# Performance work log

Hardware: AMD Instinct MI355X
Metric: run time of the kernel (lower is better)

The kernel has to match this reference:

```python
import jax, jax.numpy as jnp
import numpy as np

N_NODES = 100000
N_EDGES = 1600000
DIM_IN = 165
DIM_HID = 128


def setup_inputs() -> dict:
    key = jax.random.key(0)
    ks = jax.random.split(key, 8)
    x = jax.random.normal(ks[0], (N_NODES, DIM_IN), dtype=jnp.float32)
    edge_index = jax.random.randint(ks[1], (2, N_EDGES), 0, N_NODES, dtype=jnp.int64)
    s1 = 1.0 / np.sqrt(DIM_IN)
    s2 = 1.0 / np.sqrt(DIM_HID)
    # PyG GraphConv: lin_rel (with bias) applied to aggregated neighbors,
    # lin_root (no bias) applied to self features.
    W_rel1 = jax.random.uniform(ks[2], (DIM_HID, DIM_IN), jnp.float32, -s1, s1)
    b_rel1 = jax.random.uniform(ks[3], (DIM_HID,), jnp.float32, -s1, s1)
    W_root1 = jax.random.uniform(ks[4], (DIM_HID, DIM_IN), jnp.float32, -s1, s1)
    W_rel2 = jax.random.uniform(ks[5], (1, DIM_HID), jnp.float32, -s2, s2)
    b_rel2 = jax.random.uniform(ks[6], (1,), jnp.float32, -s2, s2)
    W_root2 = jax.random.uniform(ks[7], (1, DIM_HID), jnp.float32, -s2, s2)
    return {"x": x, "edge_index": edge_index,
            "W_rel1": W_rel1, "b_rel1": b_rel1, "W_root1": W_root1,
            "W_rel2": W_rel2, "b_rel2": b_rel2, "W_root2": W_root2}


def _graph_conv(x, src, dst, W_rel, b_rel, W_root):
    # agg[i] = sum_{(j->i) in E} x[j]  (add aggregation, source_to_target flow)
    agg = jax.ops.segment_sum(x[src], dst, num_segments=N_NODES)
    return agg @ W_rel.T + b_rel + x @ W_root.T


def reference(x, edge_index, W_rel1, b_rel1, W_root1, W_rel2, b_rel2, W_root2):
    src, dst = edge_index[0], edge_index[1]
    h = _graph_conv(x, src, dst, W_rel1, b_rel1, W_root1)
    h = jax.nn.relu(h)
    # dropout p=0.1 is identity in eval mode (deterministic reference)
    out = _graph_conv(h, src, dst, W_rel2, b_rel2, W_root2)
    return jax.nn.sigmoid(out)  # [N_NODES, 1]
```

## Files before the change

kernel.cpp:

```cpp
#include <hip/hip_runtime.h>
#include <hip/hip_bf16.h>
#include <math.h>

#define N_NODES 100000
#define N_EDGES 1600000
#define DIM_IN 165
#define DIM_HID 128
#define K_PAD 192
#define NBUCK 391
#define EPB 16384
#define NHB 98
#define CAP 6144

typedef __attribute__((ext_vector_type(8))) short short8v;
typedef __attribute__((ext_vector_type(4))) float f32x4;

__global__ void k_detect(const int* __restrict__ e32, int* __restrict__ flag,
                         int* __restrict__ gcount) {
    int t = threadIdx.x;
    if (t == 0) {
        int z = 0;
        for (int k = 0; k < 16; ++k) z |= e32[2 * k + 1];
        flag[0] = (z == 0) ? 1 : 0;
    }
    if (t < NBUCK) gcount[t] = 0;
}

__global__ void k_histB(const int* __restrict__ e32, const int* __restrict__ flag,
                        int* __restrict__ gcount, int* __restrict__ blockBase) {
    __shared__ int lc[NBUCK];
    int t = threadIdx.x;
    for (int i = t; i < NBUCK; i += 256) lc[i] = 0;
    __syncthreads();
    int isI64 = flag[0];
    int base = blockIdx.x * EPB;
    int lim = base + EPB; if (lim > N_EDGES) lim = N_EDGES;
    const long long* e64 = (const long long*)e32;
    for (int i = base + t; i < lim; i += 256) {
        int d = isI64 ? (int)e64[N_EDGES + i] : e32[N_EDGES + i];
        atomicAdd(&lc[d >> 8], 1);
    }
    __syncthreads();
    for (int b = t; b < NBUCK; b += 256)
        blockBase[blockIdx.x * NBUCK + b] = atomicAdd(&gcount[b], lc[b]);
}

__global__ void k_scanb(const int* __restrict__ gcount, int* __restrict__ bucketStart,
                        int* __restrict__ row_ptr) {
    __shared__ int s[512];
    int t = threadIdx.x;
    s[t] = (t < NBUCK) ? gcount[t] : 0;
    __syncthreads();
    for (int o = 1; o < 512; o <<= 1) {
        int v = s[t]; int a = (t >= o) ? s[t - o] : 0;
        __syncthreads(); s[t] = v + a; __syncthreads();
    }
    if (t < NBUCK) bucketStart[t + 1] = s[t];
    if (t == 0) { bucketStart[0] = 0; row_ptr[N_NODES] = N_EDGES; }
}

__global__ void k_scatterB(const int* __restrict__ e32, const int* __restrict__ flag,
                           const int* __restrict__ bucketStart, const int* __restrict__ blockBase,
                           int2* __restrict__ pairs) {
    __shared__ int lcur[NBUCK];
    int t = threadIdx.x;
    for (int b = t; b < NBUCK; b += 256)
        lcur[b] = bucketStart[b] + blockBase[blockIdx.x * NBUCK + b];
    __syncthreads();
    int isI64 = flag[0];
    int base = blockIdx.x * EPB;
    int lim = base + EPB; if (lim > N_EDGES) lim = N_EDGES;
    const long long* e64 = (const long long*)e32;
    for (int i = base + t; i < lim; i += 256) {
        int s, d;
        if (isI64) { s = (int)e64[i]; d = (int)e64[N_EDGES + i]; }
        else       { s = e32[i];      d = e32[N_EDGES + i]; }
        int pos = atomicAdd(&lcur[d >> 8], 1);
        pairs[pos] = make_int2(s, d);
    }
}

__global__ void k_sortB(const int2* __restrict__ pairs, const int* __restrict__ bucketStart,
                        int* __restrict__ row_ptr, int* __restrict__ esrc) {
    __shared__ int srcb[CAP];
    __shared__ int cnt[256];
    __shared__ int scn[256];
    int t = threadIdx.x;
    int b = blockIdx.x;
    int s0 = bucketStart[b], s1 = bucketStart[b + 1];
    int n = s1 - s0; if (n > CAP) n = CAP;
    cnt[t] = 0;
    __syncthreads();
    for (int i = t; i < n; i += 256) {
        int2 p = pairs[s0 + i];
        int ld = p.y & 255;
        srcb[i] = p.x | (ld << 20);
        atomicAdd(&cnt[ld], 1);
    }
    __syncthreads();
    scn[t] = cnt[t];
    __syncthreads();
    for (int o = 1; o < 256; o <<= 1) {
        int v = scn[t]; int a = (t >= o) ? scn[t - o] : 0;
        __syncthreads(); scn[t] = v + a; __syncthreads();
    }
    int excl = scn[t] - cnt[t];
    int node = b * 256 + t;
    if (node < N_NODES) row_ptr[node] = s0 + excl;
    __syncthreads();
    cnt[t] = excl;
    __syncthreads();
    for (int i = t; i < n; i += 256) {
        int v = srcb[i];
        int ld = v >> 20;
        int r = atomicAdd(&cnt[ld], 1);
        esrc[s0 + r] = v & 0xFFFFF;
    }
}

__global__ void k_prepw(const float* __restrict__ Wrel1, const float* __restrict__ Wroot1,
                        unsigned short* __restrict__ Wpk) {
    int idx = blockIdx.x * 256 + threadIdx.x;
    if (idx < (K_PAD / 8) * 256 * 8) {
        int j = idx & 7;
        int n = (idx >> 3) & 255;
        int p = idx >> 11;
        int k = p * 8 + j;
        float v = 0.f;
        if (k < DIM_IN) v = (n < 128) ? Wrel1[n * DIM_IN + k] : Wroot1[(n - 128) * DIM_IN + k];
        unsigned u = __float_as_uint(v);
        u += 0x7FFFu + ((u >> 16) & 1u);
        Wpk[idx] = (unsigned short)(u >> 16);
    }
}

__launch_bounds__(256, 4)
__global__ void k_gemm_mfma(const float* __restrict__ x, const unsigned short* __restrict__ Wpk,
                            unsigned short* __restrict__ y_rel, float* __restrict__ y_root) {
    __shared__ unsigned short lh[32][232];
    __shared__ unsigned short ll[32][232];
    int tid = threadIdx.x;
    int base = blockIdx.x * 32;

    const float4* xg = (const float4*)(x + (size_t)base * DIM_IN);
    for (int i = tid; i < 1320; i += 256) {
        float4 v = xg[i];
        int fi = i * 4;
        #pragma unroll
        for (int e = 0; e < 4; ++e) {
            int idx = fi + e;
            int r = idx / DIM_IN;
            int k = idx - r * DIM_IN;
            float f = (e == 0) ? v.x : (e == 1) ? v.y : (e == 2) ? v.z : v.w;
            unsigned u = __float_as_uint(f);
            unsigned short hi = (unsigned short)(u >> 16);
            float fhi = __uint_as_float(u & 0xFFFF0000u);
            float lo = f - fhi;
            unsigned short lob = (unsigned short)(__float_as_uint(lo) >> 16);
            lh[r][k] = hi;
            ll[r][k] = lob;
        }
    }
    for (int i = tid; i < 32 * (K_PAD - DIM_IN); i += 256) {
        int r = i / (K_PAD - DIM_IN);
        int k = DIM_IN + (i - r * (K_PAD - DIM_IN));
        lh[r][k] = 0; ll[r][k] = 0;
    }
    __syncthreads();

    int w = tid >> 6, l = tid & 63;
    int rowg = w & 1;
    int colh = w >> 1;
    int m = l & 15, kg = l >> 4;
    int arow = rowg * 16 + m;

    f32x4 acc[8];
    #pragma unroll
    for (int t = 0; t < 8; ++t) acc[t] = (f32x4){0.f, 0.f, 0.f, 0.f};

    const short8v* ap_h = (const short8v*)(&lh[arow][0]);
    const short8v* ap_l = (const short8v*)(&ll[arow][0]);
    const short8v* bp   = (const short8v*)Wpk;
    int bidx = kg * 256 + colh * 128 + m;

    #pragma unroll
    for (int kc = 0; kc < 6; ++kc) {
        short8v ah = ap_h[kc * 4 + kg];
        short8v al = ap_l[kc * 4 + kg];
        short8v bfrag[8];
        #pragma unroll
        for (int t = 0; t < 8; ++t) bfrag[t] = bp[bidx + kc * 1024 + t * 16];
        #pragma unroll
        for (int t = 0; t < 8; ++t)
            acc[t] = __builtin_amdgcn_mfma_f32_16x16x32_bf16(ah, bfrag[t], acc[t], 0, 0, 0);
        #pragma unroll
        for (int t = 0; t < 8; ++t)
            acc[t] = __builtin_amdgcn_mfma_f32_16x16x32_bf16(al, bfrag[t], acc[t], 0, 0, 0);
    }

    int orow = base + rowg * 16 + kg * 4;
    if (colh == 0) {
        #pragma unroll
        for (int t = 0; t < 8; ++t) {
            #pragma unroll
            for (int q = 0; q < 4; ++q) {
                unsigned u = __float_as_uint(acc[t][q]);
                u += 0x7FFFu + ((u >> 16) & 1u);
                y_rel[(size_t)(orow + q) * 128 + t * 16 + m] = (unsigned short)(u >> 16);
            }
        }
    } else {
        #pragma unroll
        for (int t = 0; t < 8; ++t) {
            #pragma unroll
            for (int q = 0; q < 4; ++q)
                y_root[(size_t)(orow + q) * 128 + t * 16 + m] = acc[t][q];
        }
    }
}

__launch_bounds__(256, 8)
__global__ void k_agg(const unsigned short* __restrict__ y_rel, const float* __restrict__ y_root,
                      const int* __restrict__ row_ptr, const int* __restrict__ esrc,
                      const float* __restrict__ b_rel1, const float* __restrict__ W_rel2,
                      const float* __restrict__ W_root2,
                      float* __restrict__ s_out, float* __restrict__ r_out) {
    int node = blockIdx.x * 4 + (threadIdx.x >> 6);
    int lane = threadIdx.x & 63;
    int li = lane & 15;
    int qid = lane >> 4;
    const uint4* yr = (const uint4*)y_rel;

    int e0 = row_ptr[node], e1 = row_ptr[node + 1];
    float a0 = 0.f, a1 = 0.f, a2 = 0.f, a3 = 0.f;
    float a4 = 0.f, a5 = 0.f, a6 = 0.f, a7 = 0.f;

    for (int eb = e0; eb < e1; eb += 64) {
        int cnt = e1 - eb; if (cnt > 64) cnt = 64;
        int ed = (eb + lane < e1) ? esrc[eb + lane] : 0;
        int kfull = cnt & ~3;
        for (int k = 0; k < kfull; k += 4) {
            int src = __shfl(ed, k + qid);
            uint4 v = yr[(size_t)src * 16 + li];
            a0 += __uint_as_float(v.x << 16); a1 += __uint_as_float(v.x & 0xFFFF0000u);
            a2 += __uint_as_float(v.y << 16); a3 += __uint_as_float(v.y & 0xFFFF0000u);
            a4 += __uint_as_float(v.z << 16); a5 += __uint_as_float(v.z & 0xFFFF0000u);
            a6 += __uint_as_float(v.w << 16); a7 += __uint_as_float(v.w & 0xFFFF0000u);
        }
        if (kfull < cnt) {
            int src = __shfl(ed, (kfull + qid < cnt) ? (kfull + qid) : kfull);
            if (kfull + qid < cnt) {
                uint4 v = yr[(size_t)src * 16 + li];
                a0 += __uint_as_float(v.x << 16); a1 += __uint_as_float(v.x & 0xFFFF0000u);
                a2 += __uint_as_float(v.y << 16); a3 += __uint_as_float(v.y & 0xFFFF0000u);
                a4 += __uint_as_float(v.z << 16); a5 += __uint_as_float(v.z & 0xFFFF0000u);
                a6 += __uint_as_float(v.w << 16); a7 += __uint_as_float(v.w & 0xFFFF0000u);
            }
        }
    }
    #pragma unroll
    for (int o = 16; o <= 32; o <<= 1) {
        a0 += __shfl_xor(a0, o); a1 += __shfl_xor(a1, o);
        a2 += __shfl_xor(a2, o); a3 += __shfl_xor(a3, o);
        a4 += __shfl_xor(a4, o); a5 += __shfl_xor(a5, o);
        a6 += __shfl_xor(a6, o); a7 += __shfl_xor(a7, o);
    }

    const float4* bb = (const float4*)(b_rel1 + 8 * li);
    const float4* rt = (const float4*)(y_root + (size_t)node * 128 + 8 * li);
    const float4* w2 = (const float4*)(W_rel2 + 8 * li);
    const float4* wo = (const float4*)(W_root2 + 8 * li);
    float4 b0 = bb[0], b1 = bb[1];
    float4 r0 = rt[0], r1 = rt[1];
    float4 p0 = w2[0], p1 = w2[1];
    float4 q0 = wo[0], q1 = wo[1];
    float h0 = fmaxf(a0 + b0.x + r0.x, 0.f), h1 = fmaxf(a1 + b0.y + r0.y, 0.f);
    float h2 = fmaxf(a2 + b0.z + r0.z, 0.f), h3 = fmaxf(a3 + b0.w + r0.w, 0.f);
    float h4 = fmaxf(a4 + b1.x + r1.x, 0.f), h5 = fmaxf(a5 + b1.y + r1.y, 0.f);
    float h6 = fmaxf(a6 + b1.z + r1.z, 0.f), h7 = fmaxf(a7 + b1.w + r1.w, 0.f);
    float sd = h0 * p0.x + h1 * p0.y + h2 * p0.z + h3 * p0.w
             + h4 * p1.x + h5 * p1.y + h6 * p1.z + h7 * p1.w;
    float rd = h0 * q0.x + h1 * q0.y + h2 * q0.z + h3 * q0.w
             + h4 * q1.x + h5 * q1.y + h6 * q1.z + h7 * q1.w;
    #pragma unroll
    for (int o = 1; o <= 8; o <<= 1) {
        sd += __shfl_xor(sd, o);
        rd += __shfl_xor(rd, o);
    }
    if (lane == 0) { s_out[node] = sd; r_out[node] = rd; }
}

__launch_bounds__(256, 8)
__global__ void k_final(const float* __restrict__ s_in, const float* __restrict__ r_in,
                        const int* __restrict__ row_ptr, const int* __restrict__ esrc,
                        const float* __restrict__ b_rel2, float* __restrict__ out) {
    int node = blockIdx.x * 4 + (threadIdx.x >> 6);
    int lane = threadIdx.x & 63;
    int e0 = row_ptr[node], e1 = row_ptr[node + 1];
    float sum = 0.f;
    for (int eb = e0; eb < e1; eb += 64) {
        if (eb + lane < e1) sum += s_in[esrc[eb + lane]];
    }
    #pragma unroll
    for (int o = 1; o <= 32; o <<= 1) sum += __shfl_xor(sum, o);
    if (lane == 0) {
        float z = sum + b_rel2[0] + r_in[node];
        out[node] = 1.f / (1.f + expf(-z));
    }
}

extern "C" void kernel_launch(void* const* d_in, const int* in_sizes, int n_in,
                              void* d_out, int out_size, void* d_ws, size_t ws_size,
                              hipStream_t stream) {
    const float* x      = (const float*)d_in[0];
    const int*   eidx   = (const int*)d_in[1];
    const float* Wrel1  = (const float*)d_in[2];
    const float* brel1  = (const float*)d_in[3];
    const float* Wroot1 = (const float*)d_in[4];
    const float* Wrel2  = (const float*)d_in[5];
    const float* brel2  = (const float*)d_in[6];
    const float* Wroot2 = (const float*)d_in[7];
    float* out = (float*)d_out;

    char* basep = (char*)d_ws;
    size_t off = 0;
    auto alloc = [&](size_t bytes) -> void* {
        off = (off + 511) & ~(size_t)511;
        void* r = basep + off;
        off += bytes;
        return r;
    };
    int*   flag        = (int*)alloc(4);
    unsigned short* Wpk = (unsigned short*)alloc((size_t)(K_PAD / 8) * 256 * 8 * 2);
    int*   row_ptr     = (int*)alloc((size_t)(N_NODES + 1) * 4);
    int*   esrc        = (int*)alloc((size_t)N_EDGES * 4);
    float* s_buf       = (float*)alloc((size_t)N_NODES * 4);
    float* r_buf       = (float*)alloc((size_t)N_NODES * 4);
    int*   bucketStart = (int*)alloc((size_t)(NBUCK + 1) * 4);
    int*   gcount      = (int*)alloc((size_t)NBUCK * 4);
    size_t union_base = (off + 511) & ~(size_t)511;
    off = union_base;
    int2*  pairs     = (int2*)alloc((size_t)N_EDGES * 8);
    int*   blockBase = (int*)alloc((size_t)NHB * NBUCK * 4);
    off = union_base;
    unsigned short* y_rel  = (unsigned short*)alloc((size_t)N_NODES * DIM_HID * 2);
    float*          y_root = (float*)alloc((size_t)N_NODES * DIM_HID * 4);

    hipLaunchKernelGGL(k_detect,   dim3(1),     dim3(512), 0, stream, eidx, flag, gcount);
    hipLaunchKernelGGL(k_histB,    dim3(NHB),   dim3(256), 0, stream, eidx, flag, gcount, blockBase);
    hipLaunchKernelGGL(k_scanb,    dim3(1),     dim3(512), 0, stream, gcount, bucketStart, row_ptr);
    hipLaunchKernelGGL(k_scatterB, dim3(NHB),   dim3(256), 0, stream, eidx, flag, bucketStart, blockBase, pairs);
    hipLaunchKernelGGL(k_sortB,    dim3(NBUCK), dim3(256), 0, stream, pairs, bucketStart, row_ptr, esrc);
    hipLaunchKernelGGL(k_prepw,    dim3(192),   dim3(256), 0, stream, Wrel1, Wroot1, Wpk);
    hipLaunchKernelGGL(k_gemm_mfma,dim3(3125),  dim3(256), 0, stream, x, Wpk, y_rel, y_root);
    hipLaunchKernelGGL(k_agg,      dim3(25000), dim3(256), 0, stream, y_rel, y_root, row_ptr, esrc,
                       brel1, Wrel2, Wroot2, s_buf, r_buf);
    hipLaunchKernelGGL(k_final,    dim3(25000), dim3(256), 0, stream, s_buf, r_buf, row_ptr, esrc,
                       brel2, out);
}
```

Baseline: 324.1 us.

## Merge init kernels, restage GEMM x loads, unroll aggregation, thread-per-node final

```diff
diff --git a/kernel.cpp b/kernel.cpp
--- a/kernel.cpp
+++ b/kernel.cpp
@@ -15,15 +15,31 @@
 typedef __attribute__((ext_vector_type(8))) short short8v;
 typedef __attribute__((ext_vector_type(4))) float f32x4;
 
-__global__ void k_detect(const int* __restrict__ e32, int* __restrict__ flag,
-                         int* __restrict__ gcount) {
-    int t = threadIdx.x;
-    if (t == 0) {
-        int z = 0;
-        for (int k = 0; k < 16; ++k) z |= e32[2 * k + 1];
-        flag[0] = (z == 0) ? 1 : 0;
-    }
-    if (t < NBUCK) gcount[t] = 0;
+__global__ void k_init(const int* __restrict__ e32, int* __restrict__ flag,
+                       int* __restrict__ gcount,
+                       const float* __restrict__ Wrel1, const float* __restrict__ Wroot1,
+                       unsigned short* __restrict__ Wpk) {
+    int b = blockIdx.x;
+    int t = threadIdx.x;
+    if (b == 0) {
+        if (t == 0) {
+            int z = 0;
+            for (int k = 0; k < 16; ++k) z |= e32[2 * k + 1];
+            flag[0] = (z == 0) ? 1 : 0;
+        }
+        for (int i = t; i < NBUCK; i += 256) gcount[i] = 0;
+    } else {
+        int idx = (b - 1) * 256 + t;
+        int j = idx & 7;
+        int n = (idx >> 3) & 255;
+        int p = idx >> 11;
+        int k = p * 8 + j;
+        float v = 0.f;
+        if (k < DIM_IN) v = (n < 128) ? Wrel1[n * DIM_IN + k] : Wroot1[(n - 128) * DIM_IN + k];
+        unsigned u = __float_as_uint(v);
+        u += 0x7FFFu + ((u >> 16) & 1u);
+        Wpk[idx] = (unsigned short)(u >> 16);
+    }
 }
 
 __global__ void k_histB(const int* __restrict__ e32, const int* __restrict__ flag,
@@ -118,22 +134,6 @@
     }
 }
 
-__global__ void k_prepw(const float* __restrict__ Wrel1, const float* __restrict__ Wroot1,
-                        unsigned short* __restrict__ Wpk) {
-    int idx = blockIdx.x * 256 + threadIdx.x;
-    if (idx < (K_PAD / 8) * 256 * 8) {
-        int j = idx & 7;
-        int n = (idx >> 3) & 255;
-        int p = idx >> 11;
-        int k = p * 8 + j;
-        float v = 0.f;
-        if (k < DIM_IN) v = (n < 128) ? Wrel1[n * DIM_IN + k] : Wroot1[(n - 128) * DIM_IN + k];
-        unsigned u = __float_as_uint(v);
-        u += 0x7FFFu + ((u >> 16) & 1u);
-        Wpk[idx] = (unsigned short)(u >> 16);
-    }
-}
-
 __launch_bounds__(256, 4)
 __global__ void k_gemm_mfma(const float* __restrict__ x, const unsigned short* __restrict__ Wpk,
                             unsigned short* __restrict__ y_rel, float* __restrict__ y_root) {
@@ -141,34 +141,33 @@
     __shared__ unsigned short ll[32][232];
     int tid = threadIdx.x;
     int base = blockIdx.x * 32;
-
-    const float4* xg = (const float4*)(x + (size_t)base * DIM_IN);
-    for (int i = tid; i < 1320; i += 256) {
-        float4 v = xg[i];
-        int fi = i * 4;
-        #pragma unroll
-        for (int e = 0; e < 4; ++e) {
-            int idx = fi + e;
-            int r = idx / DIM_IN;
-            int k = idx - r * DIM_IN;
-            float f = (e == 0) ? v.x : (e == 1) ? v.y : (e == 2) ? v.z : v.w;
-            unsigned u = __float_as_uint(f);
-            unsigned short hi = (unsigned short)(u >> 16);
-            float fhi = __uint_as_float(u & 0xFFFF0000u);
-            float lo = f - fhi;
-            unsigned short lob = (unsigned short)(__float_as_uint(lo) >> 16);
-            lh[r][k] = hi;
-            ll[r][k] = lob;
-        }
-    }
-    for (int i = tid; i < 32 * (K_PAD - DIM_IN); i += 256) {
-        int r = i / (K_PAD - DIM_IN);
-        int k = DIM_IN + (i - r * (K_PAD - DIM_IN));
-        lh[r][k] = 0; ll[r][k] = 0;
-    }
-    __syncthreads();
-
     int w = tid >> 6, l = tid & 63;
+
+    {
+        const float* xb = x + (size_t)base * DIM_IN;
+        #pragma unroll
+        for (int rr = 0; rr < 8; ++rr) {
+            int r = w * 8 + rr;
+            const float* rp = xb + (size_t)r * DIM_IN;
+            #pragma unroll
+            for (int s = 0; s < 3; ++s) {
+                int k = s * 64 + l;
+                if (s < 2 || k < DIM_IN) {
+                    float f = rp[k];
+                    unsigned u = __float_as_uint(f);
+                    unsigned short hi = (unsigned short)(u >> 16);
+                    float fhi = __uint_as_float(u & 0xFFFF0000u);
+                    float lo = f - fhi;
+                    lh[r][k] = hi;
+                    ll[r][k] = (unsigned short)(__float_as_uint(lo) >> 16);
+                } else {
+                    if (k < K_PAD) { lh[r][k] = 0; ll[r][k] = 0; }
+                }
+            }
+        }
+    }
+    __syncthreads();
+
     int rowg = w & 1;
     int colh = w >> 1;
     int m = l & 15, kg = l >> 4;
@@ -232,38 +231,49 @@
     const uint4* yr = (const uint4*)y_rel;
 
     int e0 = row_ptr[node], e1 = row_ptr[node + 1];
-    float a0 = 0.f, a1 = 0.f, a2 = 0.f, a3 = 0.f;
-    float a4 = 0.f, a5 = 0.f, a6 = 0.f, a7 = 0.f;
+    float2 c0 = {0.f, 0.f}, c1 = {0.f, 0.f}, c2 = {0.f, 0.f}, c3 = {0.f, 0.f};
+
+#define ACC4(v)                                                                   \
+    { c0.x += __uint_as_float((v).x << 16); c0.y += __uint_as_float((v).x & 0xFFFF0000u); \
+      c1.x += __uint_as_float((v).y << 16); c1.y += __uint_as_float((v).y & 0xFFFF0000u); \
+      c2.x += __uint_as_float((v).z << 16); c2.y += __uint_as_float((v).z & 0xFFFF0000u); \
+      c3.x += __uint_as_float((v).w << 16); c3.y += __uint_as_float((v).w & 0xFFFF0000u); }
 
     for (int eb = e0; eb < e1; eb += 64) {
         int cnt = e1 - eb; if (cnt > 64) cnt = 64;
         int ed = (eb + lane < e1) ? esrc[eb + lane] : 0;
-        int kfull = cnt & ~3;
-        for (int k = 0; k < kfull; k += 4) {
-            int src = __shfl(ed, k + qid);
-            uint4 v = yr[(size_t)src * 16 + li];
-            a0 += __uint_as_float(v.x << 16); a1 += __uint_as_float(v.x & 0xFFFF0000u);
-            a2 += __uint_as_float(v.y << 16); a3 += __uint_as_float(v.y & 0xFFFF0000u);
-            a4 += __uint_as_float(v.z << 16); a5 += __uint_as_float(v.z & 0xFFFF0000u);
-            a6 += __uint_as_float(v.w << 16); a7 += __uint_as_float(v.w & 0xFFFF0000u);
-        }
-        if (kfull < cnt) {
-            int src = __shfl(ed, (kfull + qid < cnt) ? (kfull + qid) : kfull);
-            if (kfull + qid < cnt) {
-                uint4 v = yr[(size_t)src * 16 + li];
-                a0 += __uint_as_float(v.x << 16); a1 += __uint_as_float(v.x & 0xFFFF0000u);
-                a2 += __uint_as_float(v.y << 16); a3 += __uint_as_float(v.y & 0xFFFF0000u);
-                a4 += __uint_as_float(v.z << 16); a5 += __uint_as_float(v.z & 0xFFFF0000u);
-                a6 += __uint_as_float(v.w << 16); a7 += __uint_as_float(v.w & 0xFFFF0000u);
+        int k = 0;
+        for (; k + 8 <= cnt; k += 8) {
+            int sA = __shfl(ed, k + qid);
+            int sB = __shfl(ed, k + 4 + qid);
+            uint4 vA = yr[(size_t)sA * 16 + li];
+            uint4 vB = yr[(size_t)sB * 16 + li];
+            ACC4(vA); ACC4(vB);
+        }
+        if (k + 4 <= cnt) {
+            int sA = __shfl(ed, k + qid);
+            uint4 vA = yr[(size_t)sA * 16 + li];
+            ACC4(vA);
+            k += 4;
+        }
+        if (k < cnt) {
+            int rem = cnt - k;
+            int idx = k + ((qid < rem) ? qid : (rem - 1));
+            int sA = __shfl(ed, idx);
+            if (qid < rem) {
+                uint4 vA = yr[(size_t)sA * 16 + li];
+                ACC4(vA);
             }
         }
     }
+#undef ACC4
+
     #pragma unroll
     for (int o = 16; o <= 32; o <<= 1) {
-        a0 += __shfl_xor(a0, o); a1 += __shfl_xor(a1, o);
-        a2 += __shfl_xor(a2, o); a3 += __shfl_xor(a3, o);
-        a4 += __shfl_xor(a4, o); a5 += __shfl_xor(a5, o);
-        a6 += __shfl_xor(a6, o); a7 += __shfl_xor(a7, o);
+        c0.x += __shfl_xor(c0.x, o); c0.y += __shfl_xor(c0.y, o);
+        c1.x += __shfl_xor(c1.x, o); c1.y += __shfl_xor(c1.y, o);
+        c2.x += __shfl_xor(c2.x, o); c2.y += __shfl_xor(c2.y, o);
+        c3.x += __shfl_xor(c3.x, o); c3.y += __shfl_xor(c3.y, o);
     }
 
     const float4* bb = (const float4*)(b_rel1 + 8 * li);
@@ -274,10 +284,10 @@
     float4 r0 = rt[0], r1 = rt[1];
     float4 p0 = w2[0], p1 = w2[1];
     float4 q0 = wo[0], q1 = wo[1];
-    float h0 = fmaxf(a0 + b0.x + r0.x, 0.f), h1 = fmaxf(a1 + b0.y + r0.y, 0.f);
-    float h2 = fmaxf(a2 + b0.z + r0.z, 0.f), h3 = fmaxf(a3 + b0.w + r0.w, 0.f);
-    float h4 = fmaxf(a4 + b1.x + r1.x, 0.f), h5 = fmaxf(a5 + b1.y + r1.y, 0.f);
-    float h6 = fmaxf(a6 + b1.z + r1.z, 0.f), h7 = fmaxf(a7 + b1.w + r1.w, 0.f);
+    float h0 = fmaxf(c0.x + b0.x + r0.x, 0.f), h1 = fmaxf(c0.y + b0.y + r0.y, 0.f);
+    float h2 = fmaxf(c1.x + b0.z + r0.z, 0.f), h3 = fmaxf(c1.y + b0.w + r0.w, 0.f);
+    float h4 = fmaxf(c2.x + b1.x + r1.x, 0.f), h5 = fmaxf(c2.y + b1.y + r1.y, 0.f);
+    float h6 = fmaxf(c3.x + b1.z + r1.z, 0.f), h7 = fmaxf(c3.y + b1.w + r1.w, 0.f);
     float sd = h0 * p0.x + h1 * p0.y + h2 * p0.z + h3 * p0.w
              + h4 * p1.x + h5 * p1.y + h6 * p1.z + h7 * p1.w;
     float rd = h0 * q0.x + h1 * q0.y + h2 * q0.z + h3 * q0.w
@@ -290,22 +300,21 @@
     if (lane == 0) { s_out[node] = sd; r_out[node] = rd; }
 }
 
-__launch_bounds__(256, 8)
 __global__ void k_final(const float* __restrict__ s_in, const float* __restrict__ r_in,
                         const int* __restrict__ row_ptr, const int* __restrict__ esrc,
                         const float* __restrict__ b_rel2, float* __restrict__ out) {
-    int node = blockIdx.x * 4 + (threadIdx.x >> 6);
-    int lane = threadIdx.x & 63;
-    int e0 = row_ptr[node], e1 = row_ptr[node + 1];
-    float sum = 0.f;
-    for (int eb = e0; eb < e1; eb += 64) {
-        if (eb + lane < e1) sum += s_in[esrc[eb + lane]];
-    }
-    #pragma unroll
-    for (int o = 1; o <= 32; o <<= 1) sum += __shfl_xor(sum, o);
-    if (lane == 0) {
-        float z = sum + b_rel2[0] + r_in[node];
-        out[node] = 1.f / (1.f + expf(-z));
+    int i = blockIdx.x * blockDim.x + threadIdx.x;
+    if (i < N_NODES) {
+        int e0 = row_ptr[i], e1 = row_ptr[i + 1];
+        float s0 = 0.f, s1 = 0.f;
+        int e = e0;
+        for (; e + 1 < e1; e += 2) {
+            s0 += s_in[esrc[e]];
+            s1 += s_in[esrc[e + 1]];
+        }
+        if (e < e1) s0 += s_in[esrc[e]];
+        float z = s0 + s1 + b_rel2[0] + r_in[i];
+        out[i] = 1.f / (1.f + expf(-z));
     }
 }
 
@@ -346,15 +355,15 @@
     unsigned short* y_rel  = (unsigned short*)alloc((size_t)N_NODES * DIM_HID * 2);
     float*          y_root = (float*)alloc((size_t)N_NODES * DIM_HID * 4);
 
-    hipLaunchKernelGGL(k_detect,   dim3(1),     dim3(512), 0, stream, eidx, flag, gcount);
+    hipLaunchKernelGGL(k_init,     dim3(193),   dim3(256), 0, stream, eidx, flag, gcount,
+                       Wrel1, Wroot1, Wpk);
     hipLaunchKernelGGL(k_histB,    dim3(NHB),   dim3(256), 0, stream, eidx, flag, gcount, blockBase);
     hipLaunchKernelGGL(k_scanb,    dim3(1),     dim3(512), 0, stream, gcount, bucketStart, row_ptr);
     hipLaunchKernelGGL(k_scatterB, dim3(NHB),   dim3(256), 0, stream, eidx, flag, bucketStart, blockBase, pairs);
     hipLaunchKernelGGL(k_sortB,    dim3(NBUCK), dim3(256), 0, stream, pairs, bucketStart, row_ptr, esrc);
-    hipLaunchKernelGGL(k_prepw,    dim3(192),   dim3(256), 0, stream, Wrel1, Wroot1, Wpk);
     hipLaunchKernelGGL(k_gemm_mfma,dim3(3125),  dim3(256), 0, stream, x, Wpk, y_rel, y_root);
     hipLaunchKernelGGL(k_agg,      dim3(25000), dim3(256), 0, stream, y_rel, y_root, row_ptr, esrc,
                        brel1, Wrel2, Wroot2, s_buf, r_buf);
-    hipLaunchKernelGGL(k_final,    dim3(25000), dim3(256), 0, stream, s_buf, r_buf, row_ptr, esrc,
+    hipLaunchKernelGGL(k_final,    dim3(391),   dim3(256), 0, stream, s_buf, r_buf, row_ptr, esrc,
                        brel2, out);
 }
```

After: 309.0 us. 1.05x faster.
